# Performance work log

Measured on AMD Instinct MI355X. Metric: run time of the kernel, lower is better.

Reference implementation:

```python
import jax, jax.numpy as jnp
import numpy as np
import math

B, T, C, H, DFF = 4, 2048, 1024, 16, 4096
HD = C // H
EPS = 1e-5


def _layernorm(x, g, b):
    mu = jnp.mean(x, axis=-1, keepdims=True)
    var = jnp.var(x, axis=-1, keepdims=True)
    return (x - mu) * jax.lax.rsqrt(var + EPS) * g + b


def _new_gelu(x):
    # 0.5*x*(1+tanh(sqrt(2/pi)*(x+0.044715*x^3)))
    c = math.sqrt(2.0 / math.pi)
    return 0.5 * x * (1.0 + jnp.tanh(c * (x + 0.044715 * x ** 3)))


def setup_inputs() -> dict:
    key = jax.random.key(0)
    ks = jax.random.split(key, 12)
    s = lambda fan_in: 1.0 / math.sqrt(fan_in)
    return {
        "x": jax.random.normal(ks[0], (B, T, C), jnp.float32),
        "ln1_g": jnp.ones((C,), jnp.float32),
        "ln1_b": jnp.zeros((C,), jnp.float32),
        "w_qkv": jax.random.normal(ks[1], (C, 3 * C), jnp.float32) * s(C),
        "b_qkv": jnp.zeros((3 * C,), jnp.float32),
        "w_o": jax.random.normal(ks[2], (C, C), jnp.float32) * s(C),
        "b_o": jnp.zeros((C,), jnp.float32),
        "ln2_g": jnp.ones((C,), jnp.float32),
        "ln2_b": jnp.zeros((C,), jnp.float32),
        "w_fc": jax.random.normal(ks[3], (C, DFF), jnp.float32) * s(C),
        "b_fc": jnp.zeros((DFF,), jnp.float32),
        "w_proj": jax.random.normal(ks[4], (DFF, C), jnp.float32) * s(DFF),
        "b_proj": jnp.zeros((C,), jnp.float32),
    }


def reference(x, ln1_g, ln1_b, w_qkv, b_qkv, w_o, b_o, ln2_g, ln2_b, w_fc, b_fc, w_proj, b_proj):
    # --- attention sub-block ---
    h = _layernorm(x, ln1_g, ln1_b)
    qkv = h @ w_qkv + b_qkv                                  # (B,T,3C)
    q, k, v = jnp.split(qkv, 3, axis=-1)
    q = q.reshape(B, T, H, HD).transpose(0, 2, 1, 3)          # (B,H,T,hd)
    k = k.reshape(B, T, H, HD).transpose(0, 2, 1, 3)
    v = v.reshape(B, T, H, HD).transpose(0, 2, 1, 3)
    scores = jnp.einsum("bhqd,bhkd->bhqk", q, k) / math.sqrt(HD)
    causal = jnp.tril(jnp.ones((T, T), jnp.bool_))            # (T,T)
    scores = jnp.where(causal[None, None], scores, -jnp.inf)
    probs = jax.nn.softmax(scores, axis=-1)
    attn = jnp.einsum("bhqk,bhkd->bhqd", probs, v)
    attn = attn.transpose(0, 2, 1, 3).reshape(B, T, C)
    x = x + attn @ w_o + b_o
    # --- MLP sub-block ---
    h2 = _layernorm(x, ln2_g, ln2_b)
    x = x + _new_gelu(h2 @ w_fc + b_fc) @ w_proj + b_proj
    return x
```

## Files before the change

kernel.cpp:

```cpp
#include <hip/hip_runtime.h>
#include <hip/hip_bf16.h>

using bf16 = __hip_bfloat16;
typedef __attribute__((ext_vector_type(8))) short bf16x8;
typedef __attribute__((ext_vector_type(4))) float f32x4;
typedef __attribute__((ext_vector_type(16))) float f32x16;

#define LOG2E 1.4426950408889634f

__device__ inline short f2b(float f) {
  __hip_bfloat16 h = __float2bfloat16(f);
  return *reinterpret_cast<short*>(&h);
}
__device__ inline float b2f(short s) {
  unsigned int u = ((unsigned int)(unsigned short)s) << 16;
  float f;
  __builtin_memcpy(&f, &u, 4);
  return f;
}
__device__ inline unsigned pk2(float a, float b) {
  return (unsigned)(unsigned short)f2b(a) |
         ((unsigned)(unsigned short)f2b(b) << 16);
}

__global__ __launch_bounds__(256) void transpose_cast_kernel(
    const float* __restrict__ in, bf16* __restrict__ out, int K, int N) {
  __shared__ float tile[32][33];
  int tx = threadIdx.x & 31;
  int ty = threadIdx.x >> 5;
  int n0 = blockIdx.x * 32, k0 = blockIdx.y * 32;
#pragma unroll
  for (int i = 0; i < 4; i++)
    tile[ty + i * 8][tx] = in[(size_t)(k0 + ty + i * 8) * N + n0 + tx];
  __syncthreads();
#pragma unroll
  for (int i = 0; i < 4; i++)
    out[(size_t)(n0 + ty + i * 8) * K + k0 + tx] =
        __float2bfloat16(tile[tx][ty + i * 8]);
}

__global__ __launch_bounds__(256) void transpose_v_kernel(
    const bf16* __restrict__ qkv, bf16* __restrict__ vt) {
  __shared__ short tile[64][66];
  const int bh = blockIdx.y;
  const int b = bh >> 4, h = bh & 15;
  const int t0 = blockIdx.x * 64;
  const int tid = threadIdx.x;
  const int r = tid >> 3, c8 = (tid & 7) * 8;
#pragma unroll
  for (int p = 0; p < 2; p++) {
    int t = r + p * 32;
    bf16x8 v = *(const bf16x8*)&qkv[(size_t)(b * 2048 + t0 + t) * 3072 + 2048 +
                                    h * 64 + c8];
#pragma unroll
    for (int i = 0; i < 8; i++) tile[t][c8 + i] = v[i];
  }
  __syncthreads();
#pragma unroll
  for (int p = 0; p < 2; p++) {
    int d = r + p * 32;
    int tt = c8;
    bf16x8 o;
#pragma unroll
    for (int i = 0; i < 8; i++) o[i] = tile[tt + i][d];
    *(bf16x8*)&vt[(size_t)(bh * 64 + d) * 2048 + t0 + tt] = o;
  }
}

__global__ __launch_bounds__(256) void ln_kernel(
    const float* __restrict__ x, const float* __restrict__ g,
    const float* __restrict__ b, bf16* __restrict__ out) {
  int row = blockIdx.x;
  const float4 v = ((const float4*)(x + (size_t)row * 1024))[threadIdx.x];
  float s = v.x + v.y + v.z + v.w;
  float ss = v.x * v.x + v.y * v.y + v.z * v.z + v.w * v.w;
#pragma unroll
  for (int off = 1; off < 64; off <<= 1) {
    s += __shfl_xor(s, off);
    ss += __shfl_xor(ss, off);
  }
  __shared__ float red[2][4];
  int w = threadIdx.x >> 6, lane = threadIdx.x & 63;
  if (lane == 0) { red[0][w] = s; red[1][w] = ss; }
  __syncthreads();
  s = red[0][0] + red[0][1] + red[0][2] + red[0][3];
  ss = red[1][0] + red[1][1] + red[1][2] + red[1][3];
  float mu = s * (1.0f / 1024.0f);
  float var = ss * (1.0f / 1024.0f) - mu * mu;
  float rstd = rsqrtf(var + 1e-5f);
  const float4 gv = ((const float4*)g)[threadIdx.x];
  const float4 bv = ((const float4*)b)[threadIdx.x];
  short4 o4;
  o4.x = f2b((v.x - mu) * rstd * gv.x + bv.x);
  o4.y = f2b((v.y - mu) * rstd * gv.y + bv.y);
  o4.z = f2b((v.z - mu) * rstd * gv.z + bv.z);
  o4.w = f2b((v.w - mu) * rstd * gv.w + bv.w);
  ((short4*)out)[(size_t)row * 256 + threadIdx.x] = o4;
}

__global__ __launch_bounds__(256) void fused_ln_kernel(
    const float* __restrict__ p0, const float* __restrict__ p1,
    const float* __restrict__ bo, const float* __restrict__ x,
    const float* __restrict__ g, const float* __restrict__ bln,
    float* __restrict__ x1, bf16* __restrict__ h2) {
  int row = blockIdx.x;
  size_t base = (size_t)row * 256 + threadIdx.x;
  float4 a = ((const float4*)p0)[base];
  float4 c = ((const float4*)p1)[base];
  float4 xr = ((const float4*)x)[base];
  float4 bo4 = ((const float4*)bo)[threadIdx.x];
  float4 v;
  v.x = a.x + c.x + xr.x + bo4.x;
  v.y = a.y + c.y + xr.y + bo4.y;
  v.z = a.z + c.z + xr.z + bo4.z;
  v.w = a.w + c.w + xr.w + bo4.w;
  ((float4*)x1)[base] = v;
  float s = v.x + v.y + v.z + v.w;
  float ss = v.x * v.x + v.y * v.y + v.z * v.z + v.w * v.w;
#pragma unroll
  for (int off = 1; off < 64; off <<= 1) {
    s += __shfl_xor(s, off);
    ss += __shfl_xor(ss, off);
  }
  __shared__ float red[2][4];
  int w = threadIdx.x >> 6, lane = threadIdx.x & 63;
  if (lane == 0) { red[0][w] = s; red[1][w] = ss; }
  __syncthreads();
  s = red[0][0] + red[0][1] + red[0][2] + red[0][3];
  ss = red[1][0] + red[1][1] + red[1][2] + red[1][3];
  float mu = s * (1.0f / 1024.0f);
  float var = ss * (1.0f / 1024.0f) - mu * mu;
  float rstd = rsqrtf(var + 1e-5f);
  const float4 gv = ((const float4*)g)[threadIdx.x];
  const float4 bv = ((const float4*)bln)[threadIdx.x];
  short4 o4;
  o4.x = f2b((v.x - mu) * rstd * gv.x + bv.x);
  o4.y = f2b((v.y - mu) * rstd * gv.y + bv.y);
  o4.z = f2b((v.z - mu) * rstd * gv.z + bv.z);
  o4.w = f2b((v.w - mu) * rstd * gv.w + bv.w);
  ((short4*)h2)[base] = o4;
}

__global__ __launch_bounds__(256) void fused_add_kernel(
    float* __restrict__ out, const float* __restrict__ q1,
    const float* __restrict__ x1, const float* __restrict__ bp, int n4) {
  for (int i = blockIdx.x * 256 + threadIdx.x; i < n4; i += gridDim.x * 256) {
    float4 a = ((const float4*)out)[i];
    float4 c = ((const float4*)q1)[i];
    float4 xr = ((const float4*)x1)[i];
    float4 b4 = ((const float4*)bp)[i & 255];
    float4 v;
    v.x = a.x + c.x + xr.x + b4.x;
    v.y = a.y + c.y + xr.y + b4.y;
    v.z = a.z + c.z + xr.z + b4.z;
    v.w = a.w + c.w + xr.w + b4.w;
    ((float4*)out)[i] = v;
  }
}

template <int EPI>
__global__ __launch_bounds__(512, 1) void gemm256_kernel(
    const bf16* __restrict__ A, const bf16* __restrict__ Bt,
    const float* __restrict__ bias, float* __restrict__ out0,
    float* __restrict__ out1, void* __restrict__ outv, int M, int N, int Kfull,
    int Ksub, int ntiles) {
  __shared__ short As[2][256 * 64];
  __shared__ short Bs[2][256 * 64];
  const int tid = threadIdx.x;
  const int lane = tid & 63, wid = tid >> 6;
  const int wr = wid >> 2, wc = wid & 3;

  const int nwg = gridDim.x;
  const int flat = blockIdx.x;
  const int sw = (flat & 7) * (nwg >> 3) + (flat >> 3);
  const int kq = sw / ntiles;
  const int tile = sw % ntiles;
  const int gy = M >> 8;
  const int bcol = tile / gy, brow = tile % gy;
  const int koff = kq * Ksub;
  const int nk = Ksub >> 6;

  const int srow = tid >> 3;
  const int schs = (tid & 7) ^ (srow & 7);

  auto stA = [&](int kt, int buf) {
#pragma unroll
    for (int r = 0; r < 4; r++) {
      const bf16* src = A + (size_t)(brow * 256 + r * 64 + srow) * Kfull +
                        koff + kt * 64 + schs * 8;
      __builtin_amdgcn_global_load_lds(
          (const __attribute__((address_space(1))) unsigned int*)src,
          (__attribute__((address_space(3))) unsigned int*)
              &As[buf][(r * 64 + wid * 8) * 64],
          16, 0, 0);
    }
  };
  auto stB = [&](int kt, int buf) {
#pragma unroll
    for (int r = 0; r < 4; r++) {
      const bf16* src = Bt + (size_t)(bcol * 256 + r * 64 + srow) * Kfull +
                        koff + kt * 64 + schs * 8;
      __builtin_amdgcn_global_load_lds(
          (const __attribute__((address_space(1))) unsigned int*)src,
          (__attribute__((address_space(3))) unsigned int*)
              &Bs[buf][(r * 64 + wid * 8) * 64],
          16, 0, 0);
    }
  };

  f32x4 acc[8][4] = {};
  bf16x8 af[4][2], bfr[4][2];

  auto rdB = [&](int cur) {
#pragma unroll
    for (int nn = 0; nn < 4; nn++)
#pragma unroll
      for (int ks = 0; ks < 2; ks++) {
        const int row = wc * 64 + nn * 16 + (lane & 15);
        const int ch = (ks * 4 + (lane >> 4)) ^ (row & 7);
        bfr[nn][ks] = *(const bf16x8*)&Bs[cur][row * 64 + ch * 8];
      }
  };
  auto rdA = [&](int cur, int mh) {
#pragma unroll
    for (int mm = 0; mm < 4; mm++)
#pragma unroll
      for (int ks = 0; ks < 2; ks++) {
        const int row = wr * 128 + mh * 64 + mm * 16 + (lane & 15);
        const int ch = (ks * 4 + (lane >> 4)) ^ (row & 7);
        af[mm][ks] = *(const bf16x8*)&As[cur][row * 64 + ch * 8];
      }
  };

  stA(0, 0);
  stB(0, 0);
  asm volatile("s_waitcnt vmcnt(0)" ::: "memory");
  __builtin_amdgcn_s_barrier();

  for (int t = 0; t < nk; t++) {
    const int cur = t & 1, nxt = cur ^ 1;
    rdB(cur);
    rdA(cur, 0);
    if (t + 1 < nk) {
      stA(t + 1, nxt);
      stB(t + 1, nxt);
    }
    __builtin_amdgcn_s_barrier();
    asm volatile("s_waitcnt lgkmcnt(0)" ::: "memory");
    __builtin_amdgcn_sched_barrier(0);
    __builtin_amdgcn_s_setprio(1);
#pragma unroll
    for (int mm = 0; mm < 4; mm++)
#pragma unroll
      for (int nn = 0; nn < 4; nn++)
#pragma unroll
        for (int ks = 0; ks < 2; ks++)
          acc[mm][nn] = __builtin_amdgcn_mfma_f32_16x16x32_bf16(
              af[mm][ks], bfr[nn][ks], acc[mm][nn], 0, 0, 0);
    __builtin_amdgcn_s_setprio(0);
    __builtin_amdgcn_s_barrier();
    rdA(cur, 1);
    asm volatile("s_waitcnt lgkmcnt(0)" ::: "memory");
    __builtin_amdgcn_sched_barrier(0);
    __builtin_amdgcn_s_setprio(1);
#pragma unroll
    for (int mm = 0; mm < 4; mm++)
#pragma unroll
      for (int nn = 0; nn < 4; nn++)
#pragma unroll
        for (int ks = 0; ks < 2; ks++)
          acc[4 + mm][nn] = __builtin_amdgcn_mfma_f32_16x16x32_bf16(
              af[mm][ks], bfr[nn][ks], acc[4 + mm][nn], 0, 0, 0);
    __builtin_amdgcn_s_setprio(0);
    if (t + 1 < nk) asm volatile("s_waitcnt vmcnt(0)" ::: "memory");
    __builtin_amdgcn_s_barrier();
  }

#pragma unroll
  for (int m = 0; m < 8; m++)
#pragma unroll
    for (int n = 0; n < 4; n++) {
      int gr0 = brow * 256 + wr * 128 + m * 16 + (lane >> 4) * 4;
      int gc = bcol * 256 + wc * 64 + n * 16 + (lane & 15);
      if constexpr (EPI == 3) {
        float* po = kq ? out1 : out0;
#pragma unroll
        for (int j = 0; j < 4; j++)
          po[(size_t)(gr0 + j) * N + gc] = acc[m][n][j];
      } else {
        float bia = bias[gc];
#pragma unroll
        for (int j = 0; j < 4; j++) {
          float v = acc[m][n][j] + bia;
          size_t idx = (size_t)(gr0 + j) * N + gc;
          if constexpr (EPI == 0) {
            ((bf16*)outv)[idx] = __float2bfloat16(v);
          } else {
            float u = 0.7978845608028654f * (v + 0.044715f * v * v * v);
            float t2 = exp2f(u * (2.0f * LOG2E));
            float th = 1.0f - 2.0f / (t2 + 1.0f);
            ((bf16*)outv)[idx] = __float2bfloat16(0.5f * v * (1.0f + th));
          }
        }
      }
    }
}

__global__ __launch_bounds__(256) void attn_kernel(
    const bf16* __restrict__ qkv, const bf16* __restrict__ vt,
    bf16* __restrict__ attn) {
  const int bh = blockIdx.x;
  const int qt = 15 - blockIdx.y;
  const int b = bh >> 4, h = bh & 15;
  const int tid = threadIdx.x, w = tid >> 6, lane = tid & 63;
  const int col = lane & 31;
  const int hi = lane >> 5;

  __shared__ short Kl[2][64 * 64];
  __shared__ short Vl[2][64 * 64];

  const int qbase = qt * 128 + w * 32;
  const int qglob = qbase + col;
  const size_t qrow = (size_t)(b * 2048 + qglob);

  bf16x8 qf[4];
#pragma unroll
  for (int dks = 0; dks < 4; dks++) {
    bf16x8 raw =
        *(const bf16x8*)&qkv[qrow * 3072 + h * 64 + dks * 16 + hi * 8];
#pragma unroll
    for (int i = 0; i < 8; i++) qf[dks][i] = f2b(b2f(raw[i]) * 0.125f);
  }

  auto stage = [&](int kt, int buf) {
    const int kv0s = kt * 64;
#pragma unroll
    for (int j = 0; j < 2; j++) {
      int c = (j * 4 + w) * 64 + lane;
      int row = c >> 3;
      int sw8 = ((c & 7) ^ (row & 7)) * 8;
      const bf16* gk =
          qkv + (size_t)(b * 2048 + kv0s + row) * 3072 + 1024 + h * 64 + sw8;
      __builtin_amdgcn_global_load_lds(
          (const __attribute__((address_space(1))) unsigned int*)gk,
          (__attribute__((address_space(3))) unsigned int*)(
              &Kl[buf][(j * 4 + w) * 512]),
          16, 0, 0);
      const bf16* gv = vt + (size_t)(bh * 64 + row) * 2048 + kv0s + sw8;
      __builtin_amdgcn_global_load_lds(
          (const __attribute__((address_space(1))) unsigned int*)gv,
          (__attribute__((address_space(3))) unsigned int*)(
              &Vl[buf][(j * 4 + w) * 512]),
          16, 0, 0);
    }
  };

  f32x16 ot[2] = {};
  float m = -1e30f, l = 0.0f;

  const int ktend = qt * 2 + 1;
  stage(0, 0);
  for (int kt = 0; kt <= ktend; kt++) {
    const int kv0 = kt * 64;
    const int cur = kt & 1;
    if (kt < ktend) {
      stage(kt + 1, cur ^ 1);
      asm volatile("s_waitcnt vmcnt(4)" ::: "memory");
    } else {
      asm volatile("s_waitcnt vmcnt(0)" ::: "memory");
    }
    __builtin_amdgcn_s_barrier();

    if (kv0 <= qbase + 31) {
      f32x16 st[2] = {};
#pragma unroll
      for (int s = 0; s < 2; s++) {
        int kvrow = s * 32 + col;
        int swz = kvrow & 7;
#pragma unroll
        for (int dks = 0; dks < 4; dks++) {
          int ch = (dks * 2 + hi) ^ swz;
          bf16x8 kf = *(const bf16x8*)&Kl[cur][kvrow * 64 + ch * 8];
          st[s] = __builtin_amdgcn_mfma_f32_32x32x16_bf16(kf, qf[dks], st[s],
                                                          0, 0, 0);
        }
      }
      if (kv0 + 63 > qbase) {
#pragma unroll
        for (int s = 0; s < 2; s++)
#pragma unroll
          for (int r = 0; r < 16; r++) {
            int kv = kv0 + s * 32 + (r & 3) + 8 * (r >> 2) + 4 * hi;
            if (kv > qglob) st[s][r] = -1e30f;
          }
      }
      float vm[16];
#pragma unroll
      for (int i = 0; i < 16; i++) vm[i] = fmaxf(st[0][i], st[1][i]);
#pragma unroll
      for (int w2 = 8; w2 >= 1; w2 >>= 1)
#pragma unroll
        for (int i = 0; i < w2; i++) vm[i] = fmaxf(vm[i], vm[i + w2]);
      float pmax = fmaxf(vm[0], __shfl_xor(vm[0], 32));
      if (!__all(pmax - m <= 8.0f)) {
        float mnew = fmaxf(m, pmax);
        float corr = exp2f((m - mnew) * LOG2E);
        m = mnew;
        l *= corr;
#pragma unroll
        for (int s = 0; s < 2; s++)
#pragma unroll
          for (int r = 0; r < 16; r++) ot[s][r] *= corr;
      }
#pragma unroll
      for (int s = 0; s < 2; s++)
#pragma unroll
        for (int r = 0; r < 16; r++)
          st[s][r] = exp2f((st[s][r] - m) * LOG2E);
      float vs[16];
#pragma unroll
      for (int i = 0; i < 16; i++) vs[i] = st[0][i] + st[1][i];
#pragma unroll
      for (int w2 = 8; w2 >= 1; w2 >>= 1)
#pragma unroll
        for (int i = 0; i < w2; i++) vs[i] += vs[i + w2];
      l += vs[0] + __shfl_xor(vs[0], 32);

#pragma unroll
      for (int sub = 0; sub < 2; sub++) {
#pragma unroll
        for (int kl = 0; kl < 2; kl++) {
          unsigned A0 = pk2(st[sub][kl * 8 + 0], st[sub][kl * 8 + 1]);
          unsigned A1 = pk2(st[sub][kl * 8 + 2], st[sub][kl * 8 + 3]);
          unsigned B0 = pk2(st[sub][kl * 8 + 4], st[sub][kl * 8 + 5]);
          unsigned B1 = pk2(st[sub][kl * 8 + 6], st[sub][kl * 8 + 7]);
          unsigned sA0 = (unsigned)__shfl_xor((int)A0, 32);
          unsigned sA1 = (unsigned)__shfl_xor((int)A1, 32);
          unsigned sB0 = (unsigned)__shfl_xor((int)B0, 32);
          unsigned sB1 = (unsigned)__shfl_xor((int)B1, 32);
          union { unsigned u[4]; bf16x8 v; } pf;
          pf.u[0] = hi ? sB0 : A0;
          pf.u[1] = hi ? sB1 : A1;
          pf.u[2] = hi ? B0 : sA0;
          pf.u[3] = hi ? B1 : sA1;
          int ks = sub * 2 + kl;
#pragma unroll
          for (int ds = 0; ds < 2; ds++) {
            int drow = ds * 32 + col;
            int ch = (ks * 2 + hi) ^ (drow & 7);
            bf16x8 vf = *(const bf16x8*)&Vl[cur][drow * 64 + ch * 8];
            ot[ds] = __builtin_amdgcn_mfma_f32_32x32x16_bf16(vf, pf.v, ot[ds],
                                                             0, 0, 0);
          }
        }
      }
    }
    __builtin_amdgcn_s_barrier();
  }

  float rl = 1.0f / l;
#pragma unroll
  for (int ds = 0; ds < 2; ds++)
#pragma unroll
    for (int j = 0; j < 4; j++) {
      ushort4 o4;
      o4.x = (unsigned short)f2b(ot[ds][4 * j + 0] * rl);
      o4.y = (unsigned short)f2b(ot[ds][4 * j + 1] * rl);
      o4.z = (unsigned short)f2b(ot[ds][4 * j + 2] * rl);
      o4.w = (unsigned short)f2b(ot[ds][4 * j + 3] * rl);
      *(ushort4*)&attn[qrow * 1024 + h * 64 + 32 * ds + 8 * j + 4 * hi] = o4;
    }
}

extern "C" void kernel_launch(void* const* d_in, const int* in_sizes, int n_in,
                              void* d_out, int out_size, void* d_ws,
                              size_t ws_size, hipStream_t stream) {
  (void)in_sizes; (void)n_in; (void)out_size; (void)ws_size;
  const float* x      = (const float*)d_in[0];
  const float* ln1_g  = (const float*)d_in[1];
  const float* ln1_b  = (const float*)d_in[2];
  const float* w_qkv  = (const float*)d_in[3];
  const float* b_qkv  = (const float*)d_in[4];
  const float* w_o    = (const float*)d_in[5];
  const float* b_o    = (const float*)d_in[6];
  const float* ln2_g  = (const float*)d_in[7];
  const float* ln2_b  = (const float*)d_in[8];
  const float* w_fc   = (const float*)d_in[9];
  const float* b_fc   = (const float*)d_in[10];
  const float* w_proj = (const float*)d_in[11];
  const float* b_proj = (const float*)d_in[12];
  float* out = (float*)d_out;

  char* ws = (char*)d_ws;
  const size_t MB = 1048576;
  float* x1     = (float*)(ws + 0);
  bf16* slotA   = (bf16*)(ws + 32 * MB);
  bf16* wt_qkv  = (bf16*)(ws + 48 * MB);
  bf16* wt_o    = (bf16*)(ws + 54 * MB);
  bf16* wt_fc   = (bf16*)(ws + 56 * MB);
  bf16* wt_proj = (bf16*)(ws + 64 * MB);
  bf16* qkvb    = (bf16*)(ws + 72 * MB);
  bf16* vtb     = (bf16*)(ws + 120 * MB);
  float* p0     = (float*)(ws + 72 * MB);
  float* p1     = (float*)(ws + 104 * MB);
  bf16* gbuf    = (bf16*)(ws + 72 * MB);
  float* q1     = (float*)(ws + 32 * MB);

  dim3 blk(256);
  transpose_cast_kernel<<<dim3(3072 / 32, 1024 / 32), blk, 0, stream>>>(
      w_qkv, wt_qkv, 1024, 3072);
  transpose_cast_kernel<<<dim3(1024 / 32, 1024 / 32), blk, 0, stream>>>(
      w_o, wt_o, 1024, 1024);
  transpose_cast_kernel<<<dim3(4096 / 32, 1024 / 32), blk, 0, stream>>>(
      w_fc, wt_fc, 1024, 4096);
  transpose_cast_kernel<<<dim3(1024 / 32, 4096 / 32), blk, 0, stream>>>(
      w_proj, wt_proj, 4096, 1024);

  ln_kernel<<<8192, blk, 0, stream>>>(x, ln1_g, ln1_b, slotA);
  gemm256_kernel<0><<<dim3(384), dim3(512), 0, stream>>>(
      slotA, wt_qkv, b_qkv, nullptr, nullptr, qkvb, 8192, 3072, 1024, 1024,
      384);
  transpose_v_kernel<<<dim3(32, 64), blk, 0, stream>>>(qkvb, vtb);
  attn_kernel<<<dim3(64, 16), blk, 0, stream>>>(qkvb, vtb, slotA);
  gemm256_kernel<3><<<dim3(256), dim3(512), 0, stream>>>(
      slotA, wt_o, nullptr, p0, p1, nullptr, 8192, 1024, 1024, 512, 128);
  fused_ln_kernel<<<8192, blk, 0, stream>>>(p0, p1, b_o, x, ln2_g, ln2_b, x1,
                                            slotA);
  gemm256_kernel<2><<<dim3(512), dim3(512), 0, stream>>>(
      slotA, wt_fc, b_fc, nullptr, nullptr, gbuf, 8192, 4096, 1024, 1024, 512);
  gemm256_kernel<3><<<dim3(256), dim3(512), 0, stream>>>(
      gbuf, wt_proj, nullptr, out, q1, nullptr, 8192, 1024, 4096, 2048, 128);
  fused_add_kernel<<<dim3(2048), blk, 0, stream>>>(out, q1, x1, b_proj,
                                                   2097152);
}
```

Baseline: 421.7 us.

## Split GEMM main loop into four quadrant phases with staggered A/B prefetch

Restructures the 256x256 bf16 GEMM main loop into four MFMA quadrant phases, each preceded by a half-sized LDS fragment read and a half-tile global-to-LDS prefetch. B is now prefetched two k-steps ahead and A one step ahead, with partial vmcnt waits instead of a full drain each iteration. LDS offsets and global base pointers are precomputed once outside the loop. The aim is to hide global load latency and spread LDS traffic between MFMA bursts, at the cost of more barriers per iteration, more live registers, and subtle buffer-reuse hazards.

After: 424.1 us. Within noise of the previous version (+0.6%).

```diff
diff --git a/kernel.cpp b/kernel.cpp
--- a/kernel.cpp
+++ b/kernel.cpp
@@ -183,68 +183,92 @@
   const int srow = tid >> 3;
   const int schs = (tid & 7) ^ (srow & 7);
 
-  auto stA = [&](int kt, int buf) {
-#pragma unroll
-    for (int r = 0; r < 4; r++) {
-      const bf16* src = A + (size_t)(brow * 256 + r * 64 + srow) * Kfull +
-                        koff + kt * 64 + schs * 8;
+  const bf16* gA[4];
+  const bf16* gB[4];
+  int dstL[4];
+#pragma unroll
+  for (int r = 0; r < 4; r++) {
+    gA[r] = A + (size_t)(brow * 256 + r * 64 + srow) * Kfull + koff + schs * 8;
+    gB[r] = Bt + (size_t)(bcol * 256 + r * 64 + srow) * Kfull + koff + schs * 8;
+    dstL[r] = (r * 64 + wid * 8) * 64;
+  }
+
+  auto stA_half = [&](int kt, int buf, int hf) {
+#pragma unroll
+    for (int rr = 0; rr < 2; rr++) {
+      const int r = hf * 2 + rr;
       __builtin_amdgcn_global_load_lds(
-          (const __attribute__((address_space(1))) unsigned int*)src,
-          (__attribute__((address_space(3))) unsigned int*)
-              &As[buf][(r * 64 + wid * 8) * 64],
+          (const __attribute__((address_space(1))) unsigned int*)(gA[r] +
+                                                                  kt * 64),
+          (__attribute__((address_space(3))) unsigned int*)&As[buf][dstL[r]],
           16, 0, 0);
     }
   };
-  auto stB = [&](int kt, int buf) {
-#pragma unroll
-    for (int r = 0; r < 4; r++) {
-      const bf16* src = Bt + (size_t)(bcol * 256 + r * 64 + srow) * Kfull +
-                        koff + kt * 64 + schs * 8;
+  auto stB_half = [&](int kt, int buf, int hf) {
+#pragma unroll
+    for (int rr = 0; rr < 2; rr++) {
+      const int r = hf * 2 + rr;
       __builtin_amdgcn_global_load_lds(
-          (const __attribute__((address_space(1))) unsigned int*)src,
-          (__attribute__((address_space(3))) unsigned int*)
-              &Bs[buf][(r * 64 + wid * 8) * 64],
+          (const __attribute__((address_space(1))) unsigned int*)(gB[r] +
+                                                                  kt * 64),
+          (__attribute__((address_space(3))) unsigned int*)&Bs[buf][dstL[r]],
           16, 0, 0);
     }
   };
 
+  int ofA[2][4][2], ofB[2][2][2];
+#pragma unroll
+  for (int qm = 0; qm < 2; qm++)
+#pragma unroll
+    for (int mm = 0; mm < 4; mm++)
+#pragma unroll
+      for (int ks = 0; ks < 2; ks++) {
+        int row = wr * 128 + qm * 64 + mm * 16 + (lane & 15);
+        int ch = (ks * 4 + (lane >> 4)) ^ (row & 7);
+        ofA[qm][mm][ks] = row * 64 + ch * 8;
+      }
+#pragma unroll
+  for (int qn = 0; qn < 2; qn++)
+#pragma unroll
+    for (int nn = 0; nn < 2; nn++)
+#pragma unroll
+      for (int ks = 0; ks < 2; ks++) {
+        int row = wc * 64 + qn * 32 + nn * 16 + (lane & 15);
+        int ch = (ks * 4 + (lane >> 4)) ^ (row & 7);
+        ofB[qn][nn][ks] = row * 64 + ch * 8;
+      }
+
   f32x4 acc[8][4] = {};
-  bf16x8 af[4][2], bfr[4][2];
-
-  auto rdB = [&](int cur) {
-#pragma unroll
-    for (int nn = 0; nn < 4; nn++)
-#pragma unroll
-      for (int ks = 0; ks < 2; ks++) {
-        const int row = wc * 64 + nn * 16 + (lane & 15);
-        const int ch = (ks * 4 + (lane >> 4)) ^ (row & 7);
-        bfr[nn][ks] = *(const bf16x8*)&Bs[cur][row * 64 + ch * 8];
-      }
-  };
-  auto rdA = [&](int cur, int mh) {
-#pragma unroll
-    for (int mm = 0; mm < 4; mm++)
-#pragma unroll
-      for (int ks = 0; ks < 2; ks++) {
-        const int row = wr * 128 + mh * 64 + mm * 16 + (lane & 15);
-        const int ch = (ks * 4 + (lane >> 4)) ^ (row & 7);
-        af[mm][ks] = *(const bf16x8*)&As[cur][row * 64 + ch * 8];
-      }
-  };
-
-  stA(0, 0);
-  stB(0, 0);
-  asm volatile("s_waitcnt vmcnt(0)" ::: "memory");
+  bf16x8 af[4][2], bf0[2][2], bf1[2][2];
+
+  stA_half(0, 0, 0);
+  stA_half(0, 0, 1);
+  stB_half(0, 0, 0);
+  stB_half(0, 0, 1);
+  if (nk > 1) {
+    stB_half(1, 1, 0);
+    stB_half(1, 1, 1);
+    asm volatile("s_waitcnt vmcnt(4)" ::: "memory");
+  } else {
+    asm volatile("s_waitcnt vmcnt(0)" ::: "memory");
+  }
   __builtin_amdgcn_s_barrier();
 
   for (int t = 0; t < nk; t++) {
     const int cur = t & 1, nxt = cur ^ 1;
-    rdB(cur);
-    rdA(cur, 0);
-    if (t + 1 < nk) {
-      stA(t + 1, nxt);
-      stB(t + 1, nxt);
-    }
+    const short* Ac = As[cur];
+    const short* Bc = Bs[cur];
+#pragma unroll
+    for (int mm = 0; mm < 4; mm++)
+#pragma unroll
+      for (int ks = 0; ks < 2; ks++)
+        af[mm][ks] = *(const bf16x8*)&Ac[ofA[0][mm][ks]];
+#pragma unroll
+    for (int nn = 0; nn < 2; nn++)
+#pragma unroll
+      for (int ks = 0; ks < 2; ks++)
+        bf0[nn][ks] = *(const bf16x8*)&Bc[ofB[0][nn][ks]];
+    if (t + 1 < nk) stA_half(t + 1, nxt, 0);
     __builtin_amdgcn_s_barrier();
     asm volatile("s_waitcnt lgkmcnt(0)" ::: "memory");
     __builtin_amdgcn_sched_barrier(0);
@@ -252,27 +276,68 @@
 #pragma unroll
     for (int mm = 0; mm < 4; mm++)
 #pragma unroll
-      for (int nn = 0; nn < 4; nn++)
+      for (int nn = 0; nn < 2; nn++)
 #pragma unroll
         for (int ks = 0; ks < 2; ks++)
           acc[mm][nn] = __builtin_amdgcn_mfma_f32_16x16x32_bf16(
-              af[mm][ks], bfr[nn][ks], acc[mm][nn], 0, 0, 0);
+              af[mm][ks], bf0[nn][ks], acc[mm][nn], 0, 0, 0);
     __builtin_amdgcn_s_setprio(0);
     __builtin_amdgcn_s_barrier();
-    rdA(cur, 1);
+#pragma unroll
+    for (int nn = 0; nn < 2; nn++)
+#pragma unroll
+      for (int ks = 0; ks < 2; ks++)
+        bf1[nn][ks] = *(const bf16x8*)&Bc[ofB[1][nn][ks]];
+    if (t + 1 < nk) stA_half(t + 1, nxt, 1);
+    __builtin_amdgcn_s_barrier();
     asm volatile("s_waitcnt lgkmcnt(0)" ::: "memory");
     __builtin_amdgcn_sched_barrier(0);
     __builtin_amdgcn_s_setprio(1);
 #pragma unroll
     for (int mm = 0; mm < 4; mm++)
 #pragma unroll
-      for (int nn = 0; nn < 4; nn++)
+      for (int nn = 0; nn < 2; nn++)
+#pragma unroll
+        for (int ks = 0; ks < 2; ks++)
+          acc[mm][2 + nn] = __builtin_amdgcn_mfma_f32_16x16x32_bf16(
+              af[mm][ks], bf1[nn][ks], acc[mm][2 + nn], 0, 0, 0);
+    __builtin_amdgcn_s_setprio(0);
+    __builtin_amdgcn_s_barrier();
+#pragma unroll
+    for (int mm = 0; mm < 4; mm++)
+#pragma unroll
+      for (int ks = 0; ks < 2; ks++)
+        af[mm][ks] = *(const bf16x8*)&Ac[ofA[1][mm][ks]];
+    if (t + 2 < nk) stB_half(t + 2, cur, 0);
+    __builtin_amdgcn_s_barrier();
+    asm volatile("s_waitcnt lgkmcnt(0)" ::: "memory");
+    __builtin_amdgcn_sched_barrier(0);
+    __builtin_amdgcn_s_setprio(1);
+#pragma unroll
+    for (int mm = 0; mm < 4; mm++)
+#pragma unroll
+      for (int nn = 0; nn < 2; nn++)
+#pragma unroll
+        for (int ks = 0; ks < 2; ks++)
+          acc[4 + mm][2 + nn] = __builtin_amdgcn_mfma_f32_16x16x32_bf16(
+              af[mm][ks], bf1[nn][ks], acc[4 + mm][2 + nn], 0, 0, 0);
+    __builtin_amdgcn_s_setprio(0);
+    __builtin_amdgcn_s_barrier();
+    if (t + 2 < nk) stB_half(t + 2, cur, 1);
+    __builtin_amdgcn_s_setprio(1);
+#pragma unroll
+    for (int mm = 0; mm < 4; mm++)
+#pragma unroll
+      for (int nn = 0; nn < 2; nn++)
 #pragma unroll
         for (int ks = 0; ks < 2; ks++)
           acc[4 + mm][nn] = __builtin_amdgcn_mfma_f32_16x16x32_bf16(
-              af[mm][ks], bfr[nn][ks], acc[4 + mm][nn], 0, 0, 0);
+              af[mm][ks], bf0[nn][ks], acc[4 + mm][nn], 0, 0, 0);
     __builtin_amdgcn_s_setprio(0);
-    if (t + 1 < nk) asm volatile("s_waitcnt vmcnt(0)" ::: "memory");
+    if (t + 2 < nk)
+      asm volatile("s_waitcnt vmcnt(4)" ::: "memory");
+    else if (t + 1 < nk)
+      asm volatile("s_waitcnt vmcnt(0)" ::: "memory");
     __builtin_amdgcn_s_barrier();
   }
 
```
